# Optimization experiments

Measured on AMD Instinct MI355X. Metric: run time of the kernel, lower is better.

The kernel has to match this reference:

```python
import jax, jax.numpy as jnp
import numpy as np

EPS = 1e-8

def squash(s, axis=-1):
    sq = jnp.sum(s * s, axis=axis, keepdims=True)
    return sq / (1.0 + sq) * s / (jnp.sqrt(sq) + EPS)

def setup_inputs() -> dict:
    key = jax.random.key(0)
    k1, k2 = jax.random.split(key)
    B, in_caps, in_dim = 256, 1152, 8
    num_caps, dim_caps = 10, 16
    x = jax.random.normal(k1, (B, in_caps, in_dim), dtype=jnp.float32)
    W = 0.01 * jax.random.normal(k2, (num_caps, in_caps, dim_caps, in_dim), dtype=jnp.float32)
    return {"x": x, "W": W}

def reference(x, W, num_routing=3):
    # u_hat: [B, num_caps, in_caps, dim_caps]
    u_hat = jnp.einsum('ncdi,bci->bncd', W, x)
    u_hat_det = jax.lax.stop_gradient(u_hat)
    B, N, C, D = u_hat.shape
    b = jnp.zeros((B, N, C, 1), dtype=u_hat.dtype)
    for _ in range(num_routing - 1):
        c = jax.nn.softmax(b, axis=1)                 # over num_caps
        s = jnp.sum(c * u_hat_det, axis=2)            # [B, N, D]
        v = squash(s)
        uv = jnp.einsum('bncd,bnd->bnc', u_hat_det, v)[..., None]
        b = b + uv
    c = jax.nn.softmax(b, axis=1)
    s = jnp.sum(c * u_hat, axis=2)
    v = squash(s)                                     # [B, N, D]
    return v
```

## Files before the change

### kernel.cpp

```cpp
#include <hip/hip_runtime.h>
#include <math.h>
#include <stdint.h>

#define B_N 256
#define C_N 1152
#define I_N 8
#define N_N 10
#define D_N 16

constexpr int C_PER    = 18;
constexpr int C_CHUNKS = C_N / C_PER;
constexpr int STAGE_C  = 3;
constexpr int N_STAGES = 6;
constexpr int BLOCK    = 256;

typedef short v8s __attribute__((ext_vector_type(8)));
typedef float v4f __attribute__((ext_vector_type(4)));

constexpr int POOL_BYTES = 32432;

constexpr size_t VSTG_FL = 16 * 16 * 164;
constexpr size_t PS_FL   = (size_t)C_CHUNKS * B_N * 160;
constexpr size_t WB_SH   = (size_t)C_N * 1280;
constexpr size_t XT_SH   = (size_t)1024 * 2304;
constexpr int    BAR_W   = 576;

#define GLD16(g, l)                                                         \
    __builtin_amdgcn_global_load_lds(                                       \
        (const uint32_t __attribute__((address_space(1)))*)(g),             \
        (uint32_t __attribute__((address_space(3)))*)(l), 16, 0, 0)

__device__ __forceinline__ void st16_sc1(float* p, v4f v) {
    asm volatile("global_store_dwordx4 %0, %1, off sc1"
                 :: "v"(p), "v"(v) : "memory");
}
__device__ __forceinline__ v4f ld16_sc1(const float* p) {
    v4f v;
    asm volatile("global_load_dwordx4 %0, %1, off sc1\n\t"
                 "s_waitcnt vmcnt(0)"
                 : "=&v"(v) : "v"(p) : "memory");
    return v;
}

__device__ __forceinline__ uint32_t cvtpk(float a, float b) {
    uint32_t r;
    asm("v_cvt_pk_bf16_f32 %0, %1, %2" : "=v"(r) : "v"(a), "v"(b));
    return r;
}
__device__ __forceinline__ float bf2f(short s) {
    return __uint_as_float(((uint32_t)(uint16_t)s) << 16);
}

__global__ __launch_bounds__(BLOCK)
void conv_all(const float* __restrict__ x, const float* __restrict__ W,
              short* __restrict__ Wb, short* __restrict__ xt,
              uint32_t* __restrict__ bar)
{
    if (blockIdx.x < 144) {
        if (blockIdx.x == 0) {
            for (int i = threadIdx.x; i < BAR_W; i += BLOCK) bar[i] = 0u;
        }
        const int c0 = blockIdx.x * 8;
        const int cc = threadIdx.x >> 5;
        const int k4 = threadIdx.x & 31;
        const float4* W4 = (const float4*)W;
        uint2* dst = (uint2*)Wb;
        for (int n = 0; n < N_N; ++n) {
            float4 v = W4[(size_t)n * 36864 + (size_t)(c0 + cc) * 32 + k4];
            dst[(((size_t)(c0 + cc) * 1280 + n * 128) >> 2) + k4] =
                make_uint2(cvtpk(v.x, v.y), cvtpk(v.z, v.w));
        }
    } else {
        const int tile  = blockIdx.x - 144;
        const int chunk = tile >> 4;
        const int btile = tile & 15;
        const int c0    = chunk * C_PER;
        const int gb0   = btile * 16;
        const float4* x4 = (const float4*)x;
        uint2* dst = (uint2*)(xt + (size_t)tile * 2304);
        #pragma unroll
        for (int it = 0; it < 3; ++it) {
            int f = threadIdx.x + BLOCK * it;
            if (f < 576) {
                int b = f / 36, r = f - b * 36;
                float4 v = x4[(size_t)(gb0 + b) * 2304 + c0 * 2 + r];
                int cp = r >> 1, i0 = (r & 1) * 4;
                dst[((cp * 128 + b * 8 + i0) >> 2)] =
                    make_uint2(cvtpk(v.x, v.y), cvtpk(v.z, v.w));
            }
        }
    }
}

__device__ __forceinline__ void gbar(uint32_t* bar, int bid, uint32_t expect)
{
    asm volatile("s_waitcnt vmcnt(0) lgkmcnt(0)" ::: "memory");
    __syncthreads();
    if (threadIdx.x == 0) {
        uint32_t a = __hip_atomic_fetch_add(&bar[(bid & 15) * 32], 1u,
                                            __ATOMIC_RELAXED,
                                            __HIP_MEMORY_SCOPE_AGENT);
        if (a == 63u) {
            uint32_t t = __hip_atomic_fetch_add(&bar[16 * 32], 1u,
                                                __ATOMIC_RELAXED,
                                                __HIP_MEMORY_SCOPE_AGENT);
            if (t == 15u) {
                #pragma unroll
                for (int i = 0; i < 17; ++i)
                    __hip_atomic_store(&bar[i * 32], 0u, __ATOMIC_RELAXED,
                                       __HIP_MEMORY_SCOPE_AGENT);
                asm volatile("s_waitcnt vmcnt(0)" ::: "memory");
                __hip_atomic_fetch_add(&bar[17 * 32], 1u, __ATOMIC_RELAXED,
                                       __HIP_MEMORY_SCOPE_AGENT);
            }
        }
        while (__hip_atomic_load(&bar[17 * 32], __ATOMIC_RELAXED,
                                 __HIP_MEMORY_SCOPE_AGENT) < expect)
            __builtin_amdgcn_s_sleep(2);
    }
    __syncthreads();
}

template <bool FIRST>
__device__ __forceinline__ void route_core(
    short* wbuf, const short* xs, float* vst, float* cfl, float* comb,
    const short* __restrict__ Wb, const float* __restrict__ vstG,
    float* __restrict__ p_s, int chunk, int btile)
{
    const int tid  = threadIdx.x;
    const int wv   = tid >> 6;
    const int lane = tid & 63;
    const int b    = lane & 15;
    const int quad = lane >> 4;
    const int gb0  = btile * 16;
    const int c0   = chunk * C_PER;

    if (!FIRST) {
        const float* src = vstG + (size_t)btile * 2624;
        const int f0 = tid;
        const int f1 = tid + 256;
        int f2 = tid + 512; f2 = (f2 < 656) ? f2 : 655;
        v4f t0, t1, t2;
        asm volatile(
            "global_load_dwordx4 %0, %3, off sc1\n\t"
            "global_load_dwordx4 %1, %4, off sc1\n\t"
            "global_load_dwordx4 %2, %5, off sc1\n\t"
            "s_waitcnt vmcnt(0)"
            : "=&v"(t0), "=&v"(t1), "=&v"(t2)
            : "v"(src + f0 * 4), "v"(src + f1 * 4), "v"(src + f2 * 4)
            : "memory");
        *(v4f*)((char*)vst + f0 * 16) = t0;
        *(v4f*)((char*)vst + f1 * 16) = t1;
        *(v4f*)((char*)vst + f2 * 16) = t2;
    }
    #pragma unroll
    for (int s0 = 0; s0 < 2; ++s0) {
        const char* src = (const char*)(Wb + (size_t)(c0 + s0 * STAGE_C) * 1280);
        char* dst = (char*)(wbuf + s0 * (STAGE_C * 1280));
        #pragma unroll
        for (int it = 0; it < 2; ++it) {
            int f = tid + BLOCK * it;
            if (f < 480) GLD16(src + f * 16, dst + f * 16);
        }
        asm volatile("" ::: "memory");
    }
    asm volatile("s_waitcnt vmcnt(2) lgkmcnt(0)" ::: "memory");
    __builtin_amdgcn_s_barrier();

    const int ncnt = (wv < 2) ? 3 : 2;
    v4f sacc[3];
    sacc[0] = (v4f){0.f, 0.f, 0.f, 0.f};
    sacc[1] = (v4f){0.f, 0.f, 0.f, 0.f};
    sacc[2] = (v4f){0.f, 0.f, 0.f, 0.f};

    for (int st = 0; st < N_STAGES; ++st) {
        const short* Ws = wbuf + (st & 1) * (STAGE_C * 1280);

        if (st >= 1 && st < N_STAGES - 1) {
            const char* src =
                (const char*)(Wb + (size_t)(c0 + (st + 1) * STAGE_C) * 1280);
            char* dst = (char*)(wbuf + ((st + 1) & 1) * (STAGE_C * 1280));
            #pragma unroll
            for (int it = 0; it < 2; ++it) {
                int f = tid + BLOCK * it;
                if (f < 480) GLD16(src + f * 16, dst + f * 16);
            }
            asm volatile("" ::: "memory");
        }

        if (!FIRST) {
            #pragma unroll
            for (int k = 0; k < 8; ++k) {
                const int idx = wv + 4 * k;
                if (idx < 30) {
                    const int c = idx / 10;
                    const int n = idx - c * 10;
                    v8s wa = {0, 0, 0, 0, 0, 0, 0, 0};
                    if (quad == 0)
                        wa = *(const v8s*)(Ws + c * 1280 + n * 128 + b * 8);
                    const v8s xb =
                        *(const v8s*)(xs + (st * STAGE_C + c) * 128 + b * 8);
                    v4f u = __builtin_amdgcn_mfma_f32_16x16x32_bf16(
                        wa, xb, (v4f){0.f, 0.f, 0.f, 0.f}, 0, 0, 0);
                    const float4 v4 =
                        *(const float4*)(vst + b * 164 + n * 16 + quad * 4);
                    float l = u[0] * v4.x + u[1] * v4.y + u[2] * v4.z + u[3] * v4.w;
                    l += __shfl_xor(l, 16);
                    l += __shfl_xor(l, 32);
                    const float e1 = __expf(l);
                    if (quad == 0) cfl[c * 163 + n * 16 + b] = e1;
                }
            }
            asm volatile("s_waitcnt lgkmcnt(0)" ::: "memory");
            __builtin_amdgcn_s_barrier();
        }

        {
            const bool valid = (quad < STAGE_C);
            const int  cl    = valid ? quad : 0;
            const v8s xq =
                *(const v8s*)(xs + (st * STAGE_C + cl) * 128 + b * 8);
            float xf[8];
            #pragma unroll
            for (int j = 0; j < 8; ++j) xf[j] = bf2f(xq[j]);

            if (FIRST) {
                union { v8s s; uint32_t u[4]; } zu;
                zu.u[0] = cvtpk(0.1f * xf[0], 0.1f * xf[1]);
                zu.u[1] = cvtpk(0.1f * xf[2], 0.1f * xf[3]);
                zu.u[2] = cvtpk(0.1f * xf[4], 0.1f * xf[5]);
                zu.u[3] = cvtpk(0.1f * xf[6], 0.1f * xf[7]);
                #pragma unroll
                for (int jj = 0; jj < 3; ++jj) {
                    if (jj < ncnt) {
                        const int n = wv + 4 * jj;
                        v8s wa = {0, 0, 0, 0, 0, 0, 0, 0};
                        if (valid)
                            wa = *(const v8s*)(Ws + cl * 1280 + n * 128 + b * 8);
                        sacc[jj] = __builtin_amdgcn_mfma_f32_16x16x32_bf16(
                            wa, zu.s, sacc[jj], 0, 0, 0);
                    }
                }
            } else {
                float Z = 0.f;
                #pragma unroll
                for (int n = 0; n < N_N; ++n) Z += cfl[cl * 163 + n * 16 + b];
                const float rzv = __builtin_amdgcn_rcpf(Z);
                #pragma unroll
                for (int jj = 0; jj < 3; ++jj) {
                    if (jj < ncnt) {
                        const int n = wv + 4 * jj;
                        const float cv = cfl[cl * 163 + n * 16 + b] * rzv;
                        union { v8s s; uint32_t u[4]; } zu;
                        zu.u[0] = cvtpk(cv * xf[0], cv * xf[1]);
                        zu.u[1] = cvtpk(cv * xf[2], cv * xf[3]);
                        zu.u[2] = cvtpk(cv * xf[4], cv * xf[5]);
                        zu.u[3] = cvtpk(cv * xf[6], cv * xf[7]);
                        v8s wa = {0, 0, 0, 0, 0, 0, 0, 0};
                        if (valid)
                            wa = *(const v8s*)(Ws + cl * 1280 + n * 128 + b * 8);
                        sacc[jj] = __builtin_amdgcn_mfma_f32_16x16x32_bf16(
                            wa, zu.s, sacc[jj], 0, 0, 0);
                    }
                }
            }
        }

        asm volatile("s_waitcnt vmcnt(0) lgkmcnt(0)" ::: "memory");
        __builtin_amdgcn_s_barrier();
    }

    #pragma unroll
    for (int jj = 0; jj < 3; ++jj) {
        if (jj < ncnt) {
            const int n = wv + 4 * jj;
            #pragma unroll
            for (int r = 0; r < 4; ++r)
                comb[b * 164 + n * 16 + quad * 4 + r] = sacc[jj][r];
        }
    }
    __syncthreads();
    #pragma unroll
    for (int it = 0; it < 3; ++it) {
        int f = tid + BLOCK * it;
        if (f < 640) {
            int e = f * 4;
            int bb = e / 160, rem = e - bb * 160;
            v4f v = *(const v4f*)(comb + bb * 164 + rem);
            st16_sc1(&p_s[((size_t)chunk * B_N + gb0 + bb) * 160 + rem], v);
        }
    }
}

__device__ __forceinline__ void reduce_core(const float* __restrict__ p_s,
                                            float* __restrict__ vstG,
                                            float* __restrict__ out,
                                            int phase, int bid)
{
    const int wv   = threadIdx.x >> 6;
    const int lane = threadIdx.x & 63;
    const int g    = wv * 1024 + bid;
    if (g >= B_N * N_N) return;
    const int q = lane & 3;
    const int h = lane >> 2;

    const float* base = p_s + (size_t)g * D_N + q * 4;
    v4f a0, a1, a2, a3;
    asm volatile(
        "global_load_dwordx4 %0, %4, off sc1\n\t"
        "global_load_dwordx4 %1, %5, off sc1\n\t"
        "global_load_dwordx4 %2, %6, off sc1\n\t"
        "global_load_dwordx4 %3, %7, off sc1\n\t"
        "s_waitcnt vmcnt(0)"
        : "=&v"(a0), "=&v"(a1), "=&v"(a2), "=&v"(a3)
        : "v"(base + (size_t)(h)      * 40960),
          "v"(base + (size_t)(h + 16) * 40960),
          "v"(base + (size_t)(h + 32) * 40960),
          "v"(base + (size_t)(h + 48) * 40960)
        : "memory");
    v4f s = a0 + a1 + a2 + a3;

    #pragma unroll
    for (int off = 4; off < 64; off <<= 1) {
        s[0] += __shfl_xor(s[0], off);
        s[1] += __shfl_xor(s[1], off);
        s[2] += __shfl_xor(s[2], off);
        s[3] += __shfl_xor(s[3], off);
    }
    float sq = s[0] * s[0] + s[1] * s[1] + s[2] * s[2] + s[3] * s[3];
    sq += __shfl_xor(sq, 1);
    sq += __shfl_xor(sq, 2);

    const float scale = (sq / (1.f + sq)) / (sqrtf(sq) + 1e-8f);
    const v4f v = {scale * s[0], scale * s[1], scale * s[2], scale * s[3]};

    if (h == 0) {
        if (phase == 2) {
            *(float4*)(&out[(size_t)g * D_N + q * 4]) =
                make_float4(v[0], v[1], v[2], v[3]);
        } else {
            const int bb = g / 10, n = g - bb * 10;
            float* vp = vstG + (size_t)(bb >> 4) * 2624 + (bb & 15) * 164 + n * 16 + q * 4;
            if (phase == 0) {
                st16_sc1(vp, v);
            } else {
                v4f o = ld16_sc1(vp);
                st16_sc1(vp, o + v);
            }
        }
    }
}

__global__ __launch_bounds__(BLOCK, 4)
void fused_route(const short* __restrict__ Wb, const short* __restrict__ xt,
                 float* __restrict__ vstG, float* __restrict__ p_s,
                 float* __restrict__ out, uint32_t* bar)
{
    __shared__ __align__(16) char pool[POOL_BYTES];
    short* wbuf = (short*)pool;
    short* xs   = (short*)(pool + 15360);
    float* vst  = (float*)(pool + 19968);
    float* cfl  = (float*)(pool + 30464);
    float* comb = (float*)pool;

    const int chunk = blockIdx.x;
    const int btile = blockIdx.y;
    const int bid   = btile * 64 + chunk;
    const int tid   = threadIdx.x;

    {
        const char* src = (const char*)(xt + (size_t)(chunk * 16 + btile) * 2304);
        #pragma unroll
        for (int it = 0; it < 2; ++it) {
            int f = tid + BLOCK * it;
            if (f < 288) GLD16(src + f * 16, (char*)xs + f * 16);
        }
        asm volatile("" ::: "memory");
    }

    route_core<true>(wbuf, xs, vst, cfl, comb, Wb, vstG, p_s, chunk, btile);
    gbar(bar, bid, 1);
    reduce_core(p_s, vstG, out, 0, bid);
    gbar(bar, bid, 2);

    #pragma unroll 1
    for (int pass = 1; pass <= 2; ++pass) {
        route_core<false>(wbuf, xs, vst, cfl, comb, Wb, vstG, p_s, chunk, btile);
        gbar(bar, bid, (uint32_t)(2 * pass + 1));
        reduce_core(p_s, vstG, out, pass == 2 ? 2 : 1, bid);
        if (pass == 1) gbar(bar, bid, 4);
    }
}

extern "C" void kernel_launch(void* const* d_in, const int* in_sizes, int n_in,
                              void* d_out, int out_size, void* d_ws, size_t ws_size,
                              hipStream_t stream)
{
    const float* x = (const float*)d_in[0];
    const float* W = (const float*)d_in[1];
    float* out  = (float*)d_out;

    float* vstG = (float*)d_ws;
    float* p_s  = vstG + VSTG_FL;
    short* Wb   = (short*)(p_s + PS_FL);
    short* xt   = Wb + WB_SH;
    uint32_t* bar = (uint32_t*)(xt + XT_SH);

    conv_all<<<dim3(144 + 1024), BLOCK, 0, stream>>>(x, W, Wb, xt, bar);
    fused_route<<<dim3(C_CHUNKS, 16), BLOCK, 0, stream>>>(Wb, xt, vstG, p_s, out, bar);
}
```

Baseline: 132.8 us.

## Replace grid-wide barrier with per-batch-tile barriers and fuse x conversion into router

The global barrier over all 1024 blocks becomes 16 independent barriers, one per batch tile of 64 blocks. To make that valid, the reduction is remapped so each batch tile's blocks reduce only their own 160 (batch, capsule) outputs. The x-to-bf16 transpose moves out of the pre-pass kernel and into the router prologue, which removes 1024 pre-pass blocks and a workspace round trip. The cost is that each router block now does the x load and convert itself with plain stores to LDS instead of async global-to-LDS loads.

```diff
diff --git a/kernel.cpp b/kernel.cpp
--- a/kernel.cpp
+++ b/kernel.cpp
@@ -22,8 +22,7 @@
 constexpr size_t VSTG_FL = 16 * 16 * 164;
 constexpr size_t PS_FL   = (size_t)C_CHUNKS * B_N * 160;
 constexpr size_t WB_SH   = (size_t)C_N * 1280;
-constexpr size_t XT_SH   = (size_t)1024 * 2304;
-constexpr int    BAR_W   = 576;
+constexpr int    BAR_W   = 16 * 64;
 
 #define GLD16(g, l)                                                         \
     __builtin_amdgcn_global_load_lds(                                       \
@@ -52,69 +51,41 @@
 }
 
 __global__ __launch_bounds__(BLOCK)
-void conv_all(const float* __restrict__ x, const float* __restrict__ W,
-              short* __restrict__ Wb, short* __restrict__ xt,
+void conv_all(const float* __restrict__ W, short* __restrict__ Wb,
               uint32_t* __restrict__ bar)
 {
-    if (blockIdx.x < 144) {
-        if (blockIdx.x == 0) {
-            for (int i = threadIdx.x; i < BAR_W; i += BLOCK) bar[i] = 0u;
-        }
-        const int c0 = blockIdx.x * 8;
-        const int cc = threadIdx.x >> 5;
-        const int k4 = threadIdx.x & 31;
-        const float4* W4 = (const float4*)W;
-        uint2* dst = (uint2*)Wb;
-        for (int n = 0; n < N_N; ++n) {
-            float4 v = W4[(size_t)n * 36864 + (size_t)(c0 + cc) * 32 + k4];
-            dst[(((size_t)(c0 + cc) * 1280 + n * 128) >> 2) + k4] =
-                make_uint2(cvtpk(v.x, v.y), cvtpk(v.z, v.w));
-        }
-    } else {
-        const int tile  = blockIdx.x - 144;
-        const int chunk = tile >> 4;
-        const int btile = tile & 15;
-        const int c0    = chunk * C_PER;
-        const int gb0   = btile * 16;
-        const float4* x4 = (const float4*)x;
-        uint2* dst = (uint2*)(xt + (size_t)tile * 2304);
-        #pragma unroll
-        for (int it = 0; it < 3; ++it) {
-            int f = threadIdx.x + BLOCK * it;
-            if (f < 576) {
-                int b = f / 36, r = f - b * 36;
-                float4 v = x4[(size_t)(gb0 + b) * 2304 + c0 * 2 + r];
-                int cp = r >> 1, i0 = (r & 1) * 4;
-                dst[((cp * 128 + b * 8 + i0) >> 2)] =
-                    make_uint2(cvtpk(v.x, v.y), cvtpk(v.z, v.w));
-            }
-        }
-    }
-}
-
-__device__ __forceinline__ void gbar(uint32_t* bar, int bid, uint32_t expect)
+    if (blockIdx.x == 0) {
+        for (int i = threadIdx.x; i < BAR_W; i += BLOCK) bar[i] = 0u;
+    }
+    const int c0 = blockIdx.x * 8;
+    const int cc = threadIdx.x >> 5;
+    const int k4 = threadIdx.x & 31;
+    const float4* W4 = (const float4*)W;
+    uint2* dst = (uint2*)Wb;
+    for (int n = 0; n < N_N; ++n) {
+        float4 v = W4[(size_t)n * 36864 + (size_t)(c0 + cc) * 32 + k4];
+        dst[(((size_t)(c0 + cc) * 1280 + n * 128) >> 2) + k4] =
+            make_uint2(cvtpk(v.x, v.y), cvtpk(v.z, v.w));
+    }
+}
+
+__device__ __forceinline__ void gbar(uint32_t* bar, int group, uint32_t expect)
 {
     asm volatile("s_waitcnt vmcnt(0) lgkmcnt(0)" ::: "memory");
     __syncthreads();
     if (threadIdx.x == 0) {
-        uint32_t a = __hip_atomic_fetch_add(&bar[(bid & 15) * 32], 1u,
-                                            __ATOMIC_RELAXED,
+        uint32_t* cnt = &bar[group * 64];
+        uint32_t* ph  = &bar[group * 64 + 32];
+        uint32_t a = __hip_atomic_fetch_add(cnt, 1u, __ATOMIC_RELAXED,
                                             __HIP_MEMORY_SCOPE_AGENT);
         if (a == 63u) {
-            uint32_t t = __hip_atomic_fetch_add(&bar[16 * 32], 1u,
-                                                __ATOMIC_RELAXED,
-                                                __HIP_MEMORY_SCOPE_AGENT);
-            if (t == 15u) {
-                #pragma unroll
-                for (int i = 0; i < 17; ++i)
-                    __hip_atomic_store(&bar[i * 32], 0u, __ATOMIC_RELAXED,
-                                       __HIP_MEMORY_SCOPE_AGENT);
-                asm volatile("s_waitcnt vmcnt(0)" ::: "memory");
-                __hip_atomic_fetch_add(&bar[17 * 32], 1u, __ATOMIC_RELAXED,
-                                       __HIP_MEMORY_SCOPE_AGENT);
-            }
-        }
-        while (__hip_atomic_load(&bar[17 * 32], __ATOMIC_RELAXED,
+            __hip_atomic_store(cnt, 0u, __ATOMIC_RELAXED,
+                               __HIP_MEMORY_SCOPE_AGENT);
+            asm volatile("s_waitcnt vmcnt(0)" ::: "memory");
+            __hip_atomic_fetch_add(ph, 1u, __ATOMIC_RELAXED,
+                                   __HIP_MEMORY_SCOPE_AGENT);
+        }
+        while (__hip_atomic_load(ph, __ATOMIC_RELAXED,
                                  __HIP_MEMORY_SCOPE_AGENT) < expect)
             __builtin_amdgcn_s_sleep(2);
     }
@@ -295,12 +266,14 @@
 __device__ __forceinline__ void reduce_core(const float* __restrict__ p_s,
                                             float* __restrict__ vstG,
                                             float* __restrict__ out,
-                                            int phase, int bid)
+                                            int phase, int chunk, int btile)
 {
     const int wv   = threadIdx.x >> 6;
     const int lane = threadIdx.x & 63;
-    const int g    = wv * 1024 + bid;
-    if (g >= B_N * N_N) return;
+    const int k    = wv * 64 + chunk;
+    if (k >= 160) return;
+    const int bb = k / 10, n = k - bb * 10;
+    const int g  = (btile * 16 + bb) * 10 + n;
     const int q = lane & 3;
     const int h = lane >> 2;
 
@@ -339,8 +312,7 @@
             *(float4*)(&out[(size_t)g * D_N + q * 4]) =
                 make_float4(v[0], v[1], v[2], v[3]);
         } else {
-            const int bb = g / 10, n = g - bb * 10;
-            float* vp = vstG + (size_t)(bb >> 4) * 2624 + (bb & 15) * 164 + n * 16 + q * 4;
+            float* vp = vstG + (size_t)btile * 2624 + bb * 164 + n * 16 + q * 4;
             if (phase == 0) {
                 st16_sc1(vp, v);
             } else {
@@ -352,7 +324,7 @@
 }
 
 __global__ __launch_bounds__(BLOCK, 4)
-void fused_route(const short* __restrict__ Wb, const short* __restrict__ xt,
+void fused_route(const float* __restrict__ x, const short* __restrict__ Wb,
                  float* __restrict__ vstG, float* __restrict__ p_s,
                  float* __restrict__ out, uint32_t* bar)
 {
@@ -365,30 +337,37 @@
 
     const int chunk = blockIdx.x;
     const int btile = blockIdx.y;
-    const int bid   = btile * 64 + chunk;
     const int tid   = threadIdx.x;
+    const int gb0   = btile * 16;
+    const int c0    = chunk * C_PER;
 
     {
-        const char* src = (const char*)(xt + (size_t)(chunk * 16 + btile) * 2304);
+        const float4* x4 = (const float4*)x;
         #pragma unroll
-        for (int it = 0; it < 2; ++it) {
+        for (int it = 0; it < 3; ++it) {
             int f = tid + BLOCK * it;
-            if (f < 288) GLD16(src + f * 16, (char*)xs + f * 16);
-        }
-        asm volatile("" ::: "memory");
+            if (f < 576) {
+                int b = f / 36, r = f - b * 36;
+                float4 v = x4[(size_t)(gb0 + b) * 2304 + c0 * 2 + r];
+                int cp = r >> 1, i0 = (r & 1) * 4;
+                *(uint2*)(xs + cp * 128 + b * 8 + i0) =
+                    make_uint2(cvtpk(v.x, v.y), cvtpk(v.z, v.w));
+            }
+        }
+        asm volatile("s_waitcnt vmcnt(0)" ::: "memory");
     }
 
     route_core<true>(wbuf, xs, vst, cfl, comb, Wb, vstG, p_s, chunk, btile);
-    gbar(bar, bid, 1);
-    reduce_core(p_s, vstG, out, 0, bid);
-    gbar(bar, bid, 2);
+    gbar(bar, btile, 1);
+    reduce_core(p_s, vstG, out, 0, chunk, btile);
+    gbar(bar, btile, 2);
 
     #pragma unroll 1
     for (int pass = 1; pass <= 2; ++pass) {
         route_core<false>(wbuf, xs, vst, cfl, comb, Wb, vstG, p_s, chunk, btile);
-        gbar(bar, bid, (uint32_t)(2 * pass + 1));
-        reduce_core(p_s, vstG, out, pass == 2 ? 2 : 1, bid);
-        if (pass == 1) gbar(bar, bid, 4);
+        gbar(bar, btile, (uint32_t)(2 * pass + 1));
+        reduce_core(p_s, vstG, out, pass == 2 ? 2 : 1, chunk, btile);
+        if (pass == 1) gbar(bar, btile, 4);
     }
 }
 
@@ -403,9 +382,8 @@
     float* vstG = (float*)d_ws;
     float* p_s  = vstG + VSTG_FL;
     short* Wb   = (short*)(p_s + PS_FL);
-    short* xt   = Wb + WB_SH;
-    uint32_t* bar = (uint32_t*)(xt + XT_SH);
-
-    conv_all<<<dim3(144 + 1024), BLOCK, 0, stream>>>(x, W, Wb, xt, bar);
-    fused_route<<<dim3(C_CHUNKS, 16), BLOCK, 0, stream>>>(Wb, xt, vstG, p_s, out, bar);
-}
+    uint32_t* bar = (uint32_t*)(Wb + WB_SH);
+
+    conv_all<<<dim3(144), BLOCK, 0, stream>>>(W, Wb, bar);
+    fused_route<<<dim3(C_CHUNKS, 16), BLOCK, 0, stream>>>(x, Wb, vstG, p_s, out, bar);
+}
```

New measurement: 122.5 us. -7.8%, faster.
